# Optimization experiments

Hardware: AMD Instinct MI355X
Metric: run time of the kernel (lower is better)

The kernel has to match this reference:

```python
import jax, jax.numpy as jnp
import numpy as np

K = 20          # motif length
A = 21          # alphabet size (amino acids + stop)
U = 600         # number of profiles
NTILES, N, F, TILE = 16, 8, 6, 334
EPS = 1e-6


def setup_inputs() -> dict:
    key = jax.random.key(0)
    kx, kp, kq = jax.random.split(key, 3)
    # X: one-hot encoded translated sequence tiles (ntiles, N, f, tile_size, alphabet)
    ids = jax.random.randint(kx, (NTILES, N, F, TILE), 0, A)
    X = jax.nn.one_hot(ids, A, dtype=jnp.float32)
    # P: softmaxed profile probabilities (k, alphabet, U) -- call() expects softmaxed P
    P = jax.nn.softmax(jax.random.normal(kp, (K, A, U), dtype=jnp.float32) * 2.0, axis=1)
    # Q: background amino-acid distribution (alphabet,)
    Q = jax.nn.softmax(jax.random.normal(kq, (A,), dtype=jnp.float32))
    return {"X": X, "P": P, "Q": Q}


def reference(X, P, Q):
    # R = log(max(P / Q, eps))  -> log-odds filter, shape (k, A, U)
    R = jnp.log(jnp.maximum(P / Q[None, :, None], EPS))
    t, n, f, L0, a = X.shape
    # tf.nn.conv2d with filter (k, A, 1, U) over (tile_size, A) windows ==
    # 1D cross-correlation over length with alphabet as input channels.
    Xf = X.reshape(t * n * f, L0, a)                      # (B, W, C_in=A)
    Z = jax.lax.conv_general_dilated(
        Xf, R, window_strides=(1,), padding='VALID',
        dimension_numbers=('NWC', 'WIO', 'NWC'))          # (B, L0-k+1, U)
    Z = Z.reshape(t, n, f, L0 - K + 1, U)                 # (ntiles, N, f, L, U)
    S = jnp.max(Z, axis=(2, 3))                           # (ntiles, N, U)
    return S, R, Z
```

## Files before the change

### kernel.cpp

```cpp
#include <hip/hip_runtime.h>
#include <stdint.h>

#define NB 768
#define LTILE 334
#define LOUT 315
#define KF 20
#define AA 21
#define UU 600
#define S_SIZE 76800
#define R_SIZE 252000

#define WS_IDS_OFF 504064
#define WS_PS_OFF  (504064 + 258048)

__global__ __launch_bounds__(256) void prep_R(const float* __restrict__ P,
                                              const float* __restrict__ Q,
                                              float* __restrict__ Rout,
                                              uint16_t* __restrict__ Rb) {
  int i = blockIdx.x * 256 + threadIdx.x;
  if (i >= R_SIZE) return;
  int a = (i / UU) % AA;
  float v = logf(fmaxf(P[i] / Q[a], 1e-6f));
  Rout[i] = v;
  uint32_t x = __float_as_uint(v);
  uint32_t r = (x + 0x7fffu + ((x >> 16) & 1u)) >> 16;
  Rb[i] = (uint16_t)r;
}

__global__ __launch_bounds__(256) void prep_ids(const float* __restrict__ X,
                                                uint8_t* __restrict__ ids) {
  int b = blockIdx.x;
  for (int pos = threadIdx.x; pos < 336; pos += 256) {
    uint8_t id = 0;
    if (pos < LTILE) {
      const float* xp = X + ((size_t)b * LTILE + pos) * AA;
#pragma unroll
      for (int a = 0; a < AA; a++)
        if (xp[a] > 0.5f) id = (uint8_t)a;
    }
    ids[b * 336 + pos] = id;
  }
}

__global__ __launch_bounds__(256) void zmain(const uint16_t* __restrict__ Rb,
                                             const uint8_t* __restrict__ ids,
                                             float* __restrict__ Z,
                                             float* __restrict__ pS) {
  __shared__ uint16_t Rl[420 * 72];
  __shared__ uint8_t idl[336];
  int b = blockIdx.x;
  int u0 = blockIdx.y * 64;
  int uw = min(64, UU - u0);
  int tid = threadIdx.x;

  int nseg = uw >> 3;
  for (int i = tid; i < 420 * nseg; i += 256) {
    int row = i / nseg, seg = i - row * nseg;
    const uint4* src = (const uint4*)(Rb + row * UU + u0 + seg * 8);
    *(uint4*)(&Rl[row * 72 + seg * 8]) = *src;
  }
  for (int i = tid; i < 84; i += 256)
    ((uint32_t*)idl)[i] = ((const uint32_t*)(ids + b * 336))[i];
  __syncthreads();

  int uoct = tid >> 5;
  int lgrp = tid & 31;
  if (uoct * 8 >= uw) return;
  int uoff = uoct * 8;

  float smax[8];
#pragma unroll
  for (int k = 0; k < 8; k++) smax[k] = -3.4e38f;

  float* Zb = Z + (size_t)b * (LOUT * UU) + u0 + uoff;

  for (int jj = 0; jj < 3; jj++) {
    int l0 = jj * 128 + lgrp * 4;
    if (l0 >= LOUT) break;
    uint32_t idw[6];
#pragma unroll
    for (int d = 0; d < 6; d++)
      idw[d] = *(const uint32_t*)(&idl[l0 + 4 * d]);

    float acc[4][8];
#pragma unroll
    for (int g = 0; g < 4; g++)
#pragma unroll
      for (int k = 0; k < 8; k++) acc[g][k] = 0.0f;

#pragma unroll
    for (int w = 0; w < KF; w++) {
#pragma unroll
      for (int g = 0; g < 4; g++) {
        int p = w + g;
        uint32_t c = (idw[p >> 2] >> ((p & 3) * 8)) & 0xFFu;
        const uint4 rv = *(const uint4*)(&Rl[(w * 21 + c) * 72 + uoff]);
        acc[g][0] += __uint_as_float(rv.x << 16);
        acc[g][1] += __uint_as_float(rv.x & 0xffff0000u);
        acc[g][2] += __uint_as_float(rv.y << 16);
        acc[g][3] += __uint_as_float(rv.y & 0xffff0000u);
        acc[g][4] += __uint_as_float(rv.z << 16);
        acc[g][5] += __uint_as_float(rv.z & 0xffff0000u);
        acc[g][6] += __uint_as_float(rv.w << 16);
        acc[g][7] += __uint_as_float(rv.w & 0xffff0000u);
      }
    }
#pragma unroll
    for (int g = 0; g < 4; g++) {
      int l = l0 + g;
      if (l < LOUT) {
        float* zp = Zb + (size_t)l * UU;
        float4 a0 = make_float4(acc[g][0], acc[g][1], acc[g][2], acc[g][3]);
        float4 a1 = make_float4(acc[g][4], acc[g][5], acc[g][6], acc[g][7]);
        *(float4*)zp = a0;
        *(float4*)(zp + 4) = a1;
#pragma unroll
        for (int k = 0; k < 8; k++) smax[k] = fmaxf(smax[k], acc[g][k]);
      }
    }
  }

#pragma unroll
  for (int k = 0; k < 8; k++) {
    float v = smax[k];
#pragma unroll
    for (int off = 16; off >= 1; off >>= 1)
      v = fmaxf(v, __shfl_down(v, off, 32));
    if (lgrp == 0) pS[b * UU + u0 + uoff + k] = v;
  }
}

__global__ __launch_bounds__(256) void finalS(const float* __restrict__ pS,
                                              float* __restrict__ S) {
  int i = blockIdx.x * 256 + threadIdx.x;
  if (i >= S_SIZE) return;
  int u = i % UU;
  int tn = i / UU;
  float m = -3.4e38f;
#pragma unroll
  for (int f = 0; f < 6; f++) m = fmaxf(m, pS[(tn * 6 + f) * UU + u]);
  S[i] = m;
}

extern "C" void kernel_launch(void* const* d_in, const int* in_sizes, int n_in,
                              void* d_out, int out_size, void* d_ws, size_t ws_size,
                              hipStream_t stream) {
  const float* X = (const float*)d_in[0];
  const float* P = (const float*)d_in[1];
  const float* Q = (const float*)d_in[2];
  float* S = (float*)d_out;
  float* R = S + S_SIZE;
  float* Z = R + R_SIZE;
  uint16_t* Rb = (uint16_t*)d_ws;
  uint8_t* ids = (uint8_t*)d_ws + WS_IDS_OFF;
  float* pS = (float*)((uint8_t*)d_ws + WS_PS_OFF);

  hipLaunchKernelGGL(prep_R, dim3((R_SIZE + 255) / 256), dim3(256), 0, stream,
                     P, Q, R, Rb);
  hipLaunchKernelGGL(prep_ids, dim3(NB), dim3(256), 0, stream, X, ids);
  hipLaunchKernelGGL(zmain, dim3(NB, 10), dim3(256), 0, stream, Rb, ids, Z, pS);
  hipLaunchKernelGGL(finalS, dim3((S_SIZE + 255) / 256), dim3(256), 0, stream,
                     pS, S);
}
```

Before: 979.6 us.

## Precompute pairwise filter-row sums and index by residue digrams to halve gathers

Builds a table of summed R rows for each pair of adjacent filter positions and each residue pair, and encodes each sequence position as a digram index. The main convolution then does 10 gathered adds per output instead of 20. The grid is remapped so each block handles 8 sequences for 8 profiles, and accumulation uses packed float2 vectors. This adds a larger workspace table and a separate prep kernel, and Z stores become narrower per row, which may hurt write coalescing.

Measured after the change: 932.6 us. 1.05x faster.

```diff
diff --git a/kernel.cpp b/kernel.cpp
--- a/kernel.cpp
+++ b/kernel.cpp
@@ -10,25 +10,61 @@
 #define S_SIZE 76800
 #define R_SIZE 252000
 
-#define WS_IDS_OFF 504064
-#define WS_PS_OFF  (504064 + 258048)
+#define NDG 441
+#define NW2 10
+#define TROWS (NW2 * NDG)
+#define UCH 75
+#define BGRP 96
+
+#define WS_R2C_OFF 0
+#define WS_DIG_OFF 5292032
+#define WS_PS_OFF  (5292032 + 516096)
+
+typedef float v2f __attribute__((ext_vector_type(2)));
+
+__device__ __forceinline__ uint32_t bf16rne(float v) {
+  uint32_t x = __float_as_uint(v);
+  return (x + 0x7fffu + ((x >> 16) & 1u)) >> 16;
+}
 
 __global__ __launch_bounds__(256) void prep_R(const float* __restrict__ P,
                                               const float* __restrict__ Q,
-                                              float* __restrict__ Rout,
-                                              uint16_t* __restrict__ Rb) {
+                                              float* __restrict__ Rout) {
   int i = blockIdx.x * 256 + threadIdx.x;
   if (i >= R_SIZE) return;
   int a = (i / UU) % AA;
-  float v = logf(fmaxf(P[i] / Q[a], 1e-6f));
-  Rout[i] = v;
-  uint32_t x = __float_as_uint(v);
-  uint32_t r = (x + 0x7fffu + ((x >> 16) & 1u)) >> 16;
-  Rb[i] = (uint16_t)r;
+  Rout[i] = logf(fmaxf(P[i] / Q[a], 1e-6f));
+}
+
+__global__ __launch_bounds__(256) void prep_R2(const float* __restrict__ Rout,
+                                               uint16_t* __restrict__ R2c) {
+  int t = blockIdx.x * 256 + threadIdx.x;
+  if (t >= UCH * TROWS) return;
+  int uc = t / TROWS;
+  int i = t - uc * TROWS;
+  int w2 = i / NDG;
+  int c12 = i - w2 * NDG;
+  int c1 = c12 / AA;
+  int c2 = c12 - c1 * AA;
+  const float* pa = Rout + ((2 * w2) * AA + c1) * UU + uc * 8;
+  const float* pb = Rout + ((2 * w2 + 1) * AA + c2) * UU + uc * 8;
+  float4 a0 = *(const float4*)pa, a1 = *(const float4*)(pa + 4);
+  float4 b0 = *(const float4*)pb, b1 = *(const float4*)(pb + 4);
+  uint32_t r0 = bf16rne(a0.x + b0.x), r1 = bf16rne(a0.y + b0.y);
+  uint32_t r2 = bf16rne(a0.z + b0.z), r3 = bf16rne(a0.w + b0.w);
+  uint32_t r4 = bf16rne(a1.x + b1.x), r5 = bf16rne(a1.y + b1.y);
+  uint32_t r6 = bf16rne(a1.z + b1.z), r7 = bf16rne(a1.w + b1.w);
+  uint4 out;
+  out.x = r0 | (r1 << 16);
+  out.y = r2 | (r3 << 16);
+  out.z = r4 | (r5 << 16);
+  out.w = r6 | (r7 << 16);
+  *(uint4*)(R2c + (size_t)t * 8) = out;
 }
 
 __global__ __launch_bounds__(256) void prep_ids(const float* __restrict__ X,
-                                                uint8_t* __restrict__ ids) {
+                                                uint16_t* __restrict__ dig) {
+  __shared__ uint8_t idl[336];
   int b = blockIdx.x;
   for (int pos = threadIdx.x; pos < 336; pos += 256) {
     uint8_t id = 0;
@@ -38,71 +74,78 @@
       for (int a = 0; a < AA; a++)
         if (xp[a] > 0.5f) id = (uint8_t)a;
     }
-    ids[b * 336 + pos] = id;
-  }
-}
-
-__global__ __launch_bounds__(256) void zmain(const uint16_t* __restrict__ Rb,
-                                             const uint8_t* __restrict__ ids,
+    idl[pos] = id;
+  }
+  __syncthreads();
+  for (int p = threadIdx.x; p < 336; p += 256) {
+    uint16_t d = 0;
+    if (p < 335) d = (uint16_t)(idl[p] * AA + idl[p + 1]);
+    dig[b * 336 + p] = d;
+  }
+}
+
+__global__ __launch_bounds__(256) void zmain(const uint16_t* __restrict__ R2c,
+                                             const uint16_t* __restrict__ dig,
                                              float* __restrict__ Z,
                                              float* __restrict__ pS) {
-  __shared__ uint16_t Rl[420 * 72];
-  __shared__ uint8_t idl[336];
-  int b = blockIdx.x;
-  int u0 = blockIdx.y * 64;
-  int uw = min(64, UU - u0);
+  __shared__ __align__(16) uint16_t Tl[TROWS * 8];
+  __shared__ __align__(16) uint16_t digl[8 * 336];
+  int b0 = blockIdx.x * 8;
+  int u0 = blockIdx.y * 8;
   int tid = threadIdx.x;
 
-  int nseg = uw >> 3;
-  for (int i = tid; i < 420 * nseg; i += 256) {
-    int row = i / nseg, seg = i - row * nseg;
-    const uint4* src = (const uint4*)(Rb + row * UU + u0 + seg * 8);
-    *(uint4*)(&Rl[row * 72 + seg * 8]) = *src;
-  }
-  for (int i = tid; i < 84; i += 256)
-    ((uint32_t*)idl)[i] = ((const uint32_t*)(ids + b * 336))[i];
+  const uint16_t* Tsrc = R2c + (size_t)blockIdx.y * (TROWS * 8);
+  for (int i = tid; i < TROWS; i += 256)
+    *(uint4*)(&Tl[i * 8]) = *(const uint4*)(Tsrc + i * 8);
+  const uint32_t* dsrc = (const uint32_t*)(dig + (size_t)b0 * 336);
+  for (int i = tid; i < 1344; i += 256) ((uint32_t*)digl)[i] = dsrc[i];
   __syncthreads();
 
-  int uoct = tid >> 5;
+  int bslot = tid >> 5;
   int lgrp = tid & 31;
-  if (uoct * 8 >= uw) return;
-  int uoff = uoct * 8;
+  int b = b0 + bslot;
+  const uint16_t* dl = digl + bslot * 336;
 
   float smax[8];
 #pragma unroll
   for (int k = 0; k < 8; k++) smax[k] = -3.4e38f;
 
-  float* Zb = Z + (size_t)b * (LOUT * UU) + u0 + uoff;
+  float* Zb = Z + (size_t)b * (LOUT * UU) + u0;
 
   for (int jj = 0; jj < 3; jj++) {
     int l0 = jj * 128 + lgrp * 4;
     if (l0 >= LOUT) break;
-    uint32_t idw[6];
-#pragma unroll
-    for (int d = 0; d < 6; d++)
-      idw[d] = *(const uint32_t*)(&idl[l0 + 4 * d]);
-
-    float acc[4][8];
+    uint32_t idw[12];
+    const uint32_t* dwp = (const uint32_t*)(dl + l0);
+#pragma unroll
+    for (int d = 0; d < 6; d++) {
+      uint2 t = *(const uint2*)(dwp + 2 * d);
+      idw[2 * d] = t.x;
+      idw[2 * d + 1] = t.y;
+    }
+
+    v2f acc[4][4];
 #pragma unroll
     for (int g = 0; g < 4; g++)
 #pragma unroll
-      for (int k = 0; k < 8; k++) acc[g][k] = 0.0f;
-
-#pragma unroll
-    for (int w = 0; w < KF; w++) {
+      for (int d = 0; d < 4; d++) acc[g][d] = (v2f){0.0f, 0.0f};
+
+#pragma unroll
+    for (int w2 = 0; w2 < NW2; w2++) {
 #pragma unroll
       for (int g = 0; g < 4; g++) {
-        int p = w + g;
-        uint32_t c = (idw[p >> 2] >> ((p & 3) * 8)) & 0xFFu;
-        const uint4 rv = *(const uint4*)(&Rl[(w * 21 + c) * 72 + uoff]);
-        acc[g][0] += __uint_as_float(rv.x << 16);
-        acc[g][1] += __uint_as_float(rv.x & 0xffff0000u);
-        acc[g][2] += __uint_as_float(rv.y << 16);
-        acc[g][3] += __uint_as_float(rv.y & 0xffff0000u);
-        acc[g][4] += __uint_as_float(rv.z << 16);
-        acc[g][5] += __uint_as_float(rv.z & 0xffff0000u);
-        acc[g][6] += __uint_as_float(rv.w << 16);
-        acc[g][7] += __uint_as_float(rv.w & 0xffff0000u);
+        int r = 2 * w2 + g;
+        uint32_t wv = idw[r >> 1];
+        uint32_t c = (r & 1) ? (wv >> 16) : (wv & 0xFFFFu);
+        const uint4 rv = *(const uint4*)(&Tl[(w2 * NDG + c) * 8]);
+        v2f t0 = {__uint_as_float(rv.x << 16), __uint_as_float(rv.x & 0xffff0000u)};
+        v2f t1 = {__uint_as_float(rv.y << 16), __uint_as_float(rv.y & 0xffff0000u)};
+        v2f t2 = {__uint_as_float(rv.z << 16), __uint_as_float(rv.z & 0xffff0000u)};
+        v2f t3 = {__uint_as_float(rv.w << 16), __uint_as_float(rv.w & 0xffff0000u)};
+        acc[g][0] += t0;
+        acc[g][1] += t1;
+        acc[g][2] += t2;
+        acc[g][3] += t3;
       }
     }
 #pragma unroll
@@ -110,12 +153,18 @@
       int l = l0 + g;
       if (l < LOUT) {
         float* zp = Zb + (size_t)l * UU;
-        float4 a0 = make_float4(acc[g][0], acc[g][1], acc[g][2], acc[g][3]);
-        float4 a1 = make_float4(acc[g][4], acc[g][5], acc[g][6], acc[g][7]);
+        float4 a0 = make_float4(acc[g][0][0], acc[g][0][1], acc[g][1][0], acc[g][1][1]);
+        float4 a1 = make_float4(acc[g][2][0], acc[g][2][1], acc[g][3][0], acc[g][3][1]);
         *(float4*)zp = a0;
         *(float4*)(zp + 4) = a1;
-#pragma unroll
-        for (int k = 0; k < 8; k++) smax[k] = fmaxf(smax[k], acc[g][k]);
+        smax[0] = fmaxf(smax[0], a0.x);
+        smax[1] = fmaxf(smax[1], a0.y);
+        smax[2] = fmaxf(smax[2], a0.z);
+        smax[3] = fmaxf(smax[3], a0.w);
+        smax[4] = fmaxf(smax[4], a1.x);
+        smax[5] = fmaxf(smax[5], a1.y);
+        smax[6] = fmaxf(smax[6], a1.z);
+        smax[7] = fmaxf(smax[7], a1.w);
       }
     }
   }
@@ -126,7 +175,7 @@
 #pragma unroll
     for (int off = 16; off >= 1; off >>= 1)
       v = fmaxf(v, __shfl_down(v, off, 32));
-    if (lgrp == 0) pS[b * UU + u0 + uoff + k] = v;
+    if (lgrp == 0) pS[(size_t)b * UU + u0 + k] = v;
   }
 }
 
@@ -151,14 +200,17 @@
   float* S = (float*)d_out;
   float* R = S + S_SIZE;
   float* Z = R + R_SIZE;
-  uint16_t* Rb = (uint16_t*)d_ws;
-  uint8_t* ids = (uint8_t*)d_ws + WS_IDS_OFF;
+  uint16_t* R2c = (uint16_t*)d_ws;
+  uint16_t* digW = (uint16_t*)((uint8_t*)d_ws + WS_DIG_OFF);
   float* pS = (float*)((uint8_t*)d_ws + WS_PS_OFF);
 
   hipLaunchKernelGGL(prep_R, dim3((R_SIZE + 255) / 256), dim3(256), 0, stream,
-                     P, Q, R, Rb);
-  hipLaunchKernelGGL(prep_ids, dim3(NB), dim3(256), 0, stream, X, ids);
-  hipLaunchKernelGGL(zmain, dim3(NB, 10), dim3(256), 0, stream, Rb, ids, Z, pS);
+                     P, Q, R);
+  hipLaunchKernelGGL(prep_ids, dim3(NB), dim3(256), 0, stream, X, digW);
+  hipLaunchKernelGGL(prep_R2, dim3((UCH * TROWS + 255) / 256), dim3(256), 0,
+                     stream, R, R2c);
+  hipLaunchKernelGGL(zmain, dim3(BGRP, UCH), dim3(256), 0, stream, R2c, digW,
+                     Z, pS);
   hipLaunchKernelGGL(finalS, dim3((S_SIZE + 255) / 256), dim3(256), 0, stream,
                      pS, S);
 }
```

## Remap zmain threads so each wave writes full contiguous Z rows

Applied to the files above, without the earlier changes.

Restructures the zmain thread mapping so each lane handles one output position and an 8-wide column segment. A wave of 64 lanes now covers 8 positions by 64 columns, making Z stores contiguous across lanes. The shared table is unpadded (64 stride), sequence ids are read directly from global memory instead of LDS, and packed float2 accumulation is used. The max reduction now goes through xor shuffles plus a cross-wave LDS step, with launch bounds raised to allow 3 blocks per CU. The intent is to coalesce the dominant Z write traffic and cut register pressure. The risk is more LDS lookups per output and possible bank conflicts from the unpadded layout.

Result: faster. 804.8 us (-17.8%).

```diff
diff --git a/kernel.cpp b/kernel.cpp
--- a/kernel.cpp
+++ b/kernel.cpp
@@ -9,9 +9,12 @@
 #define UU 600
 #define S_SIZE 76800
 #define R_SIZE 252000
+#define NROWS 420
 
 #define WS_IDS_OFF 504064
-#define WS_PS_OFF  (504064 + 258048)
+#define WS_PS_OFF  (504064 + 258112)
+
+typedef float v2f __attribute__((ext_vector_type(2)));
 
 __global__ __launch_bounds__(256) void prep_R(const float* __restrict__ P,
                                               const float* __restrict__ Q,
@@ -42,91 +45,102 @@
   }
 }
 
-__global__ __launch_bounds__(256) void zmain(const uint16_t* __restrict__ Rb,
-                                             const uint8_t* __restrict__ ids,
-                                             float* __restrict__ Z,
-                                             float* __restrict__ pS) {
-  __shared__ uint16_t Rl[420 * 72];
-  __shared__ uint8_t idl[336];
+__global__ __launch_bounds__(256, 3) void zmain(const uint16_t* __restrict__ Rb,
+                                                const uint8_t* __restrict__ ids,
+                                                float* __restrict__ Z,
+                                                float* __restrict__ pS) {
+  __shared__ __align__(16) uint16_t Tl[NROWS * 64];
   int b = blockIdx.x;
   int u0 = blockIdx.y * 64;
   int uw = min(64, UU - u0);
+  int nseg = uw >> 3;
   int tid = threadIdx.x;
 
-  int nseg = uw >> 3;
-  for (int i = tid; i < 420 * nseg; i += 256) {
+  for (int i = tid; i < NROWS * nseg; i += 256) {
     int row = i / nseg, seg = i - row * nseg;
-    const uint4* src = (const uint4*)(Rb + row * UU + u0 + seg * 8);
-    *(uint4*)(&Rl[row * 72 + seg * 8]) = *src;
+    *(uint4*)(&Tl[row * 64 + seg * 8]) =
+        *(const uint4*)(Rb + row * UU + u0 + seg * 8);
   }
-  for (int i = tid; i < 84; i += 256)
-    ((uint32_t*)idl)[i] = ((const uint32_t*)(ids + b * 336))[i];
   __syncthreads();
 
-  int uoct = tid >> 5;
-  int lgrp = tid & 31;
-  if (uoct * 8 >= uw) return;
-  int uoff = uoct * 8;
+  int wave = tid >> 6;
+  int lane = tid & 63;
+  int seg = lane & 7;
+  int lrow = lane >> 3;
+  bool segok = seg < nseg;
+  const uint8_t* idb = ids + b * 336;
+  const char* Tseg = (const char*)Tl + seg * 16;
 
-  float smax[8];
+  v2f sm[4];
 #pragma unroll
-  for (int k = 0; k < 8; k++) smax[k] = -3.4e38f;
+  for (int d = 0; d < 4; d++) sm[d] = (v2f){-3.4e38f, -3.4e38f};
 
-  float* Zb = Z + (size_t)b * (LOUT * UU) + u0 + uoff;
+  for (int pass = 0; pass < 10; pass++) {
+    int l = pass * 32 + wave * 8 + lrow;
+    if (l < LOUT && segok) {
+      int al = l & ~3;
+      int sh = (l & 3) * 8;
+      const uint32_t* wp = (const uint32_t*)(idb + al);
+      uint32_t raw[6];
+#pragma unroll
+      for (int j = 0; j < 6; j++) raw[j] = wp[j];
+      uint32_t W[5];
+#pragma unroll
+      for (int j = 0; j < 5; j++)
+        W[j] = (uint32_t)((((uint64_t)raw[j + 1] << 32) | raw[j]) >> sh);
 
-  for (int jj = 0; jj < 3; jj++) {
-    int l0 = jj * 128 + lgrp * 4;
-    if (l0 >= LOUT) break;
-    uint32_t idw[6];
+      v2f acc[4];
 #pragma unroll
-    for (int d = 0; d < 6; d++)
-      idw[d] = *(const uint32_t*)(&idl[l0 + 4 * d]);
-
-    float acc[4][8];
-#pragma unroll
-    for (int g = 0; g < 4; g++)
-#pragma unroll
-      for (int k = 0; k < 8; k++) acc[g][k] = 0.0f;
+      for (int d = 0; d < 4; d++) acc[d] = (v2f){0.0f, 0.0f};
 
 #pragma unroll
-    for (int w = 0; w < KF; w++) {
+      for (int w = 0; w < KF; w++) {
+        uint32_t c = (W[w >> 2] >> ((w & 3) * 8)) & 0xFFu;
+        const uint4 rv = *(const uint4*)(Tseg + (c << 7) + w * 2688);
+        acc[0] += (v2f){__uint_as_float(rv.x << 16),
+                        __uint_as_float(rv.x & 0xffff0000u)};
+        acc[1] += (v2f){__uint_as_float(rv.y << 16),
+                        __uint_as_float(rv.y & 0xffff0000u)};
+        acc[2] += (v2f){__uint_as_float(rv.z << 16),
+                        __uint_as_float(rv.z & 0xffff0000u)};
+        acc[3] += (v2f){__uint_as_float(rv.w << 16),
+                        __uint_as_float(rv.w & 0xffff0000u)};
+      }
+
+      float* zp = Z + ((size_t)b * LOUT + l) * UU + u0 + seg * 8;
+      *(float4*)zp = make_float4(acc[0][0], acc[0][1], acc[1][0], acc[1][1]);
+      *(float4*)(zp + 4) =
+          make_float4(acc[2][0], acc[2][1], acc[3][0], acc[3][1]);
 #pragma unroll
-      for (int g = 0; g < 4; g++) {
-        int p = w + g;
-        uint32_t c = (idw[p >> 2] >> ((p & 3) * 8)) & 0xFFu;
-        const uint4 rv = *(const uint4*)(&Rl[(w * 21 + c) * 72 + uoff]);
-        acc[g][0] += __uint_as_float(rv.x << 16);
-        acc[g][1] += __uint_as_float(rv.x & 0xffff0000u);
-        acc[g][2] += __uint_as_float(rv.y << 16);
-        acc[g][3] += __uint_as_float(rv.y & 0xffff0000u);
-        acc[g][4] += __uint_as_float(rv.z << 16);
-        acc[g][5] += __uint_as_float(rv.z & 0xffff0000u);
-        acc[g][6] += __uint_as_float(rv.w << 16);
-        acc[g][7] += __uint_as_float(rv.w & 0xffff0000u);
-      }
-    }
-#pragma unroll
-    for (int g = 0; g < 4; g++) {
-      int l = l0 + g;
-      if (l < LOUT) {
-        float* zp = Zb + (size_t)l * UU;
-        float4 a0 = make_float4(acc[g][0], acc[g][1], acc[g][2], acc[g][3]);
-        float4 a1 = make_float4(acc[g][4], acc[g][5], acc[g][6], acc[g][7]);
-        *(float4*)zp = a0;
-        *(float4*)(zp + 4) = a1;
-#pragma unroll
-        for (int k = 0; k < 8; k++) smax[k] = fmaxf(smax[k], acc[g][k]);
+      for (int d = 0; d < 4; d++) {
+        sm[d][0] = fmaxf(sm[d][0], acc[d][0]);
+        sm[d][1] = fmaxf(sm[d][1], acc[d][1]);
       }
     }
   }
 
 #pragma unroll
-  for (int k = 0; k < 8; k++) {
-    float v = smax[k];
+  for (int d = 0; d < 4; d++) {
 #pragma unroll
-    for (int off = 16; off >= 1; off >>= 1)
-      v = fmaxf(v, __shfl_down(v, off, 32));
-    if (lgrp == 0) pS[b * UU + u0 + uoff + k] = v;
+    for (int off = 8; off <= 32; off <<= 1) {
+      sm[d][0] = fmaxf(sm[d][0], __shfl_xor(sm[d][0], off));
+      sm[d][1] = fmaxf(sm[d][1], __shfl_xor(sm[d][1], off));
+    }
+  }
+
+  __syncthreads();
+  float* red = (float*)Tl;
+  if (lane < 8) {
+    float* rp = red + wave * 64 + lane * 8;
+    *(float4*)rp = make_float4(sm[0][0], sm[0][1], sm[1][0], sm[1][1]);
+    *(float4*)(rp + 4) = make_float4(sm[2][0], sm[2][1], sm[3][0], sm[3][1]);
+  }
+  __syncthreads();
+  if (tid < 64 && tid < uw) {
+    float v = red[tid];
+#pragma unroll
+    for (int w2 = 1; w2 < 4; w2++) v = fmaxf(v, red[w2 * 64 + tid]);
+    pS[(size_t)b * UU + u0 + tid] = v;
   }
 }
 
```
